# Kernel tuning notes

Measured on AMD Instinct MI355X. Metric: run time of the kernel, lower is better.

The kernel has to match this reference:

```python
import jax, jax.numpy as jnp
import numpy as np

D_MODEL = 1024
D_FF = 4096
NUM_EXPERTS = 8
TOP_K = 2


def setup_inputs() -> dict:
    key = jax.random.key(0)
    ks = jax.random.split(key, 10)
    s = 0.02
    x = jax.random.normal(ks[0], (2, 1024, D_MODEL), dtype=jnp.float32)
    # router gate (nn.Linear(d_model, num_experts))
    Wr = jax.random.normal(ks[1], (D_MODEL, NUM_EXPERTS), dtype=jnp.float32) * s
    br = jnp.zeros((NUM_EXPERTS,), dtype=jnp.float32)
    # stacked expert weights
    Wg = jax.random.normal(ks[2], (NUM_EXPERTS, D_MODEL, D_FF), dtype=jnp.float32) * s
    bg = jnp.zeros((NUM_EXPERTS, D_FF), dtype=jnp.float32)
    Wu = jax.random.normal(ks[3], (NUM_EXPERTS, D_MODEL, D_FF), dtype=jnp.float32) * s
    bu = jnp.zeros((NUM_EXPERTS, D_FF), dtype=jnp.float32)
    Wd = jax.random.normal(ks[4], (NUM_EXPERTS, D_FF, D_MODEL), dtype=jnp.float32) * s
    bd = jnp.zeros((NUM_EXPERTS, D_MODEL), dtype=jnp.float32)
    return {"x": x, "Wr": Wr, "br": br, "Wg": Wg, "bg": bg,
            "Wu": Wu, "bu": bu, "Wd": Wd, "bd": bd}


def reference(x, Wr, br, Wg, bg, Wu, bu, Wd, bd):
    B, S, D = x.shape
    E = Wg.shape[0]
    xt = x.reshape(-1, D)                       # [T, d]
    T = xt.shape[0]
    # router: softmax in float32, top-k, renormalize (Mixtral-style)
    logits = xt @ Wr + br                       # [T, E]
    probs = jax.nn.softmax(logits.astype(jnp.float32), axis=-1)
    rw, sel = jax.lax.top_k(probs, TOP_K)       # [T, K]
    rw = rw / jnp.sum(rw, axis=-1, keepdims=True)
    # per-token per-expert combine weight (0 if expert not selected)
    w_full = jnp.zeros((T, E), dtype=rw.dtype).at[
        jnp.arange(T)[:, None], sel].add(rw)    # [T, E]
    # SwiGLU experts, computed densely over all tokens then masked-combined
    g = jnp.einsum('td,edf->etf', xt, Wg) + bg[:, None, :]   # [E, T, f]
    u = jnp.einsum('td,edf->etf', xt, Wu) + bu[:, None, :]
    h = jax.nn.silu(g) * u
    y = jnp.einsum('etf,efd->etd', h, Wd) + bd[:, None, :]    # [E, T, d]
    out = jnp.einsum('te,etd->td', w_full.astype(x.dtype), y)
    return out.reshape(B, S, D)
```

## Files before the change

kernel.cpp:

```cpp
#include <hip/hip_runtime.h>

typedef float floatx4 __attribute__((ext_vector_type(4)));
typedef __bf16 bf16x2 __attribute__((ext_vector_type(2)));
typedef __bf16 bf16x4 __attribute__((ext_vector_type(4)));
typedef __bf16 bf16x8 __attribute__((ext_vector_type(8)));

#define D_MODEL 1024
#define D_FF 4096
#define NE 8

__device__ __forceinline__ void gload16(const void* g, void* l) {
    __builtin_amdgcn_global_load_lds(
        (const __attribute__((address_space(1))) void*)g,
        (__attribute__((address_space(3))) void*)l, 16, 0, 0);
}

__device__ __forceinline__ int frag_off(int row, int q) {
    return row * 32 + ((q ^ ((row >> 2) & 3)) << 3);
}

__device__ __forceinline__ unsigned int pk(float lo, float hi) {
    union { bf16x2 v; unsigned int u; } c;
    c.v = bf16x2{(__bf16)lo, (__bf16)hi};
    return c.u;
}

__global__ __launch_bounds__(256) void router_kernel(
    const float* __restrict__ x, const float* __restrict__ Wr,
    const float* __restrict__ br, int* __restrict__ cnt,
    int* __restrict__ list, float* __restrict__ w_slot, int T)
{
    int wv = threadIdx.x >> 6;
    int lane = threadIdx.x & 63;
    int t = blockIdx.x * 4 + wv;
    if (t >= T) return;

    const float* xp = x + (size_t)t * D_MODEL;
    float acc[8] = {0.f,0.f,0.f,0.f,0.f,0.f,0.f,0.f};
#pragma unroll
    for (int i = 0; i < 16; ++i) {
        int d = i * 64 + lane;
        float xv = xp[d];
        float4 w0 = *(const float4*)(Wr + d * 8);
        float4 w1 = *(const float4*)(Wr + d * 8 + 4);
        acc[0] += xv * w0.x; acc[1] += xv * w0.y;
        acc[2] += xv * w0.z; acc[3] += xv * w0.w;
        acc[4] += xv * w1.x; acc[5] += xv * w1.y;
        acc[6] += xv * w1.z; acc[7] += xv * w1.w;
    }
#pragma unroll
    for (int off = 32; off >= 1; off >>= 1) {
#pragma unroll
        for (int e = 0; e < 8; ++e)
            acc[e] += __shfl_down(acc[e], off, 64);
    }
    if (lane == 0) {
        float l[8];
#pragma unroll
        for (int e = 0; e < 8; ++e) l[e] = acc[e] + br[e];
        int i0 = 0; float v0 = l[0];
#pragma unroll
        for (int e = 1; e < 8; ++e) if (l[e] > v0) { v0 = l[e]; i0 = e; }
        int i1 = -1; float v1 = -3.4e38f;
#pragma unroll
        for (int e = 0; e < 8; ++e) if (e != i0 && l[e] > v1) { v1 = l[e]; i1 = e; }
        float ex = __expf(v1 - v0);
        float w0 = 1.f / (1.f + ex);
        float w1 = ex / (1.f + ex);
        int p0 = atomicAdd(&cnt[i0], 1);
        list[i0 * T + p0] = 2 * t;
        int p1 = atomicAdd(&cnt[i1], 1);
        list[i1 * T + p1] = 2 * t + 1;
        w_slot[2 * t]     = w0;
        w_slot[2 * t + 1] = w1;
    }
}

__global__ __launch_bounds__(256) void prep_kernel(
    const float* __restrict__ Wg, const float* __restrict__ Wu,
    const float* __restrict__ Wd, const float* __restrict__ x,
    __bf16* __restrict__ Wgt, __bf16* __restrict__ Wut,
    __bf16* __restrict__ Wdt, __bf16* __restrict__ Xb)
{
    const int bid = blockIdx.x;
    const int tid = threadIdx.x;
    if (bid >= 24576) {
        int base = (bid - 24576) * 2048 + tid * 8;
        float4 v0 = *(const float4*)(x + base);
        float4 v1 = *(const float4*)(x + base + 4);
        bf16x8 o = {(__bf16)v0.x, (__bf16)v0.y, (__bf16)v0.z, (__bf16)v0.w,
                    (__bf16)v1.x, (__bf16)v1.y, (__bf16)v1.z, (__bf16)v1.w};
        *(bf16x8*)(Xb + base) = o;
        return;
    }
    const int tensor = bid >> 13;
    const int rem = bid & 8191;
    const int e = rem >> 10;
    const int tile = rem & 1023;
    const float* src; __bf16* dst; int K, N, kb, nb;
    if (tensor == 0)      { src = Wg; dst = Wgt; }
    else if (tensor == 1) { src = Wu; dst = Wut; }
    else                  { src = Wd; dst = Wdt; }
    if (tensor < 2) { K = 1024; N = 4096; kb = (tile & 15) << 6; nb = (tile >> 4) << 6; }
    else            { K = 4096; N = 1024; kb = (tile & 63) << 6; nb = (tile >> 6) << 6; }
    src += (size_t)e * K * N + (size_t)kb * N + nb;
    dst += (size_t)e * K * N + (size_t)nb * K + kb;

    __shared__ unsigned int tp[64 * 33];

    const int p  = tid >> 3;
    const int ci = tid & 7;
    const float* s0 = src + (size_t)(2 * p) * N + 4 * ci;
    float4 r0a = *(const float4*)(s0);
    float4 r0b = *(const float4*)(s0 + 32);
    float4 r1a = *(const float4*)(s0 + N);
    float4 r1b = *(const float4*)(s0 + N + 32);

    unsigned int* w0 = &tp[(4 * ci) * 33 + p];
    w0[0]  = pk(r0a.x, r1a.x);
    w0[33] = pk(r0a.y, r1a.y);
    w0[66] = pk(r0a.z, r1a.z);
    w0[99] = pk(r0a.w, r1a.w);
    unsigned int* w1 = &tp[(4 * ci + 32) * 33 + p];
    w1[0]  = pk(r0b.x, r1b.x);
    w1[33] = pk(r0b.y, r1b.y);
    w1[66] = pk(r0b.z, r1b.z);
    w1[99] = pk(r0b.w, r1b.w);
    __syncthreads();

    const int r = tid >> 2;
    const int q = tid & 3;
    const unsigned int* rp = &tp[r * 33 + q * 8];
    uint4 oa = {rp[0], rp[1], rp[2], rp[3]};
    uint4 ob = {rp[4], rp[5], rp[6], rp[7]};
    __bf16* drow = dst + (size_t)r * K + q * 16;
    *(uint4*)(drow)     = oa;
    *(uint4*)(drow + 8) = ob;
}

__global__ __launch_bounds__(256, 3) void gateup3_kernel(
    const __bf16* __restrict__ Xb, const __bf16* __restrict__ Wgt,
    const __bf16* __restrict__ Wut, const float* __restrict__ bg,
    const float* __restrict__ bu, const int* __restrict__ cnt,
    const int* __restrict__ list, __bf16* __restrict__ H, int T)
{
    const int e  = blockIdx.z;
    const int m0 = blockIdx.y * 128;
    const int n0 = blockIdx.x * 64;
    const int count = cnt[e];
    if (m0 >= count) return;

    __shared__ __bf16 ldsA[8192];
    __shared__ __bf16 ldsBg[4096];
    __shared__ __bf16 ldsBu[4096];
    __shared__ int s_entry[128];

    const int tid = threadIdx.x;
    if (tid < 128) {
        int r = m0 + tid;
        s_entry[tid] = (r < count) ? list[e * T + r] : list[e * T];
    }
    __syncthreads();

    const __bf16* asrc[4]; char* adst[4];
#pragma unroll
    for (int i = 0; i < 4; ++i) {
        int p = i * 256 + tid;
        int s = p >> 9;
        int row = (p & 511) >> 2, j = p & 3;
        int g = j ^ ((row >> 2) & 3);
        asrc[i] = Xb + (size_t)(s_entry[row] >> 1) * D_MODEL + s * 32 + g * 8;
        adst[i] = (char*)ldsA + p * 16;
    }
    const __bf16* gsrc[2]; const __bf16* usrc[2]; char* gdst[2]; char* udst[2];
#pragma unroll
    for (int i = 0; i < 2; ++i) {
        int p = i * 256 + tid;
        int s = p >> 8;
        int row = (p & 255) >> 2, j = p & 3;
        int g = j ^ ((row >> 2) & 3);
        gsrc[i] = Wgt + ((size_t)e * D_FF + n0 + row) * D_MODEL + s * 32 + g * 8;
        usrc[i] = Wut + ((size_t)e * D_FF + n0 + row) * D_MODEL + s * 32 + g * 8;
        gdst[i] = (char*)ldsBg + p * 16;
        udst[i] = (char*)ldsBu + p * 16;
    }

    const int wv = tid >> 6, lane = tid & 63;
    const int wm = wv >> 1, wn = wv & 1;
    const int q = lane >> 4, ln = lane & 15;
    int aoff[4], boff[2];
#pragma unroll
    for (int i = 0; i < 4; ++i) aoff[i] = frag_off(wm * 64 + i * 16 + ln, q);
#pragma unroll
    for (int i = 0; i < 2; ++i) boff[i] = frag_off(wn * 32 + i * 16 + ln, q);

    floatx4 accg[4][2] = {};
    floatx4 accu[4][2] = {};

    for (int k0 = 0; k0 < D_MODEL; k0 += 64) {
#pragma unroll
        for (int i = 0; i < 4; ++i) gload16(asrc[i] + k0, adst[i]);
#pragma unroll
        for (int i = 0; i < 2; ++i) {
            gload16(gsrc[i] + k0, gdst[i]);
            gload16(usrc[i] + k0, udst[i]);
        }
        __syncthreads();

#pragma unroll
        for (int s = 0; s < 2; ++s) {
            bf16x8 af[4], bgf[2], buf[2];
#pragma unroll
            for (int i = 0; i < 4; ++i) af[i]  = *(const bf16x8*)&ldsA[s * 4096 + aoff[i]];
#pragma unroll
            for (int i = 0; i < 2; ++i) bgf[i] = *(const bf16x8*)&ldsBg[s * 2048 + boff[i]];
#pragma unroll
            for (int i = 0; i < 2; ++i) buf[i] = *(const bf16x8*)&ldsBu[s * 2048 + boff[i]];
#pragma unroll
            for (int mi = 0; mi < 4; ++mi)
#pragma unroll
                for (int ni = 0; ni < 2; ++ni) {
                    accg[mi][ni] = __builtin_amdgcn_mfma_f32_16x16x32_bf16(af[mi], bgf[ni], accg[mi][ni], 0, 0, 0);
                    accu[mi][ni] = __builtin_amdgcn_mfma_f32_16x16x32_bf16(af[mi], buf[ni], accu[mi][ni], 0, 0, 0);
                }
        }
        __syncthreads();
    }

#pragma unroll
    for (int ni = 0; ni < 2; ++ni) {
        int col = n0 + wn * 32 + ni * 16 + ln;
        float bgv = bg[e * D_FF + col];
        float buv = bu[e * D_FF + col];
#pragma unroll
        for (int mi = 0; mi < 4; ++mi) {
            int lrow0 = wm * 64 + mi * 16 + q * 4;
#pragma unroll
            for (int r = 0; r < 4; ++r) {
                int lr = lrow0 + r;
                if (m0 + lr < count) {
                    int entry = s_entry[lr];
                    float g = accg[mi][ni][r] + bgv;
                    float u = accu[mi][ni][r] + buv;
                    float h = g / (1.f + __expf(-g)) * u;
                    H[(size_t)entry * D_FF + col] = (__bf16)h;
                }
            }
        }
    }
}

__global__ __launch_bounds__(256, 3) void down3_kernel(
    const __bf16* __restrict__ H, const __bf16* __restrict__ Wdt,
    const float* __restrict__ bd, const int* __restrict__ cnt,
    const int* __restrict__ list, float* __restrict__ Y, int T)
{
    const int e  = blockIdx.z >> 2;
    const int kc = blockIdx.z & 3;
    const int m0 = blockIdx.y * 128;
    const int n0 = blockIdx.x * 128;
    const int count = cnt[e];
    if (m0 >= count) return;

    __shared__ __bf16 ldsA[8192];
    __shared__ __bf16 ldsB[8192];
    __shared__ int s_entry[128];

    const int tid = threadIdx.x;
    if (tid < 128) {
        int r = m0 + tid;
        s_entry[tid] = (r < count) ? list[e * T + r] : list[e * T];
    }
    __syncthreads();

    const int kbase = kc * (D_FF / 4);
    const __bf16* asrc[4]; const __bf16* bsrc[4];
    char* adst[4]; char* bdst[4];
#pragma unroll
    for (int i = 0; i < 4; ++i) {
        int p = i * 256 + tid;
        int s = p >> 9;
        int row = (p & 511) >> 2, j = p & 3;
        int g = j ^ ((row >> 2) & 3);
        asrc[i] = H + (size_t)s_entry[row] * D_FF + kbase + s * 32 + g * 8;
        bsrc[i] = Wdt + ((size_t)e * D_MODEL + n0 + row) * D_FF + kbase + s * 32 + g * 8;
        adst[i] = (char*)ldsA + p * 16;
        bdst[i] = (char*)ldsB + p * 16;
    }

    const int wv = tid >> 6, lane = tid & 63;
    const int wm = wv >> 1, wn = wv & 1;
    const int q = lane >> 4, ln = lane & 15;
    int aoff[4], boff[4];
#pragma unroll
    for (int i = 0; i < 4; ++i) {
        aoff[i] = frag_off(wm * 64 + i * 16 + ln, q);
        boff[i] = frag_off(wn * 64 + i * 16 + ln, q);
    }

    floatx4 acc[4][4] = {};

    for (int k0 = 0; k0 < D_FF / 4; k0 += 64) {
#pragma unroll
        for (int i = 0; i < 4; ++i) {
            gload16(asrc[i] + k0, adst[i]);
            gload16(bsrc[i] + k0, bdst[i]);
        }
        __syncthreads();

#pragma unroll
        for (int s = 0; s < 2; ++s) {
            bf16x8 af[4], bf[4];
#pragma unroll
            for (int i = 0; i < 4; ++i) af[i] = *(const bf16x8*)&ldsA[s * 4096 + aoff[i]];
#pragma unroll
            for (int i = 0; i < 4; ++i) bf[i] = *(const bf16x8*)&ldsB[s * 4096 + boff[i]];
#pragma unroll
            for (int mi = 0; mi < 4; ++mi)
#pragma unroll
                for (int ni = 0; ni < 4; ++ni)
                    acc[mi][ni] = __builtin_amdgcn_mfma_f32_16x16x32_bf16(af[mi], bf[ni], acc[mi][ni], 0, 0, 0);
        }
        __syncthreads();
    }

    const size_t kc_off = (size_t)kc * 2 * T * D_MODEL;
#pragma unroll
    for (int ni = 0; ni < 4; ++ni) {
        int col = n0 + wn * 64 + ni * 16 + ln;
        float bdv = (kc == 0) ? bd[e * D_MODEL + col] : 0.f;
#pragma unroll
        for (int mi = 0; mi < 4; ++mi) {
            int lrow0 = wm * 64 + mi * 16 + q * 4;
#pragma unroll
            for (int r = 0; r < 4; ++r) {
                int lr = lrow0 + r;
                if (m0 + lr < count) {
                    int entry = s_entry[lr];
                    Y[kc_off + (size_t)entry * D_MODEL + col] = acc[mi][ni][r] + bdv;
                }
            }
        }
    }
}

__global__ __launch_bounds__(256) void combine_kernel(
    const float* __restrict__ Y, const float* __restrict__ w_slot,
    float* __restrict__ out, int T)
{
    int idx = blockIdx.x * 256 + threadIdx.x;
    int t = idx >> 8;
    const float4* Y4 = (const float4*)Y;
    size_t r0 = (size_t)(2 * t) * 256 + (idx & 255);
    size_t r1 = r0 + 256;
    size_t ks = (size_t)2 * T * 256;
    float4 a = Y4[r0], b = Y4[r1];
#pragma unroll
    for (int kc = 1; kc < 4; ++kc) {
        float4 va = Y4[r0 + kc * ks], vb = Y4[r1 + kc * ks];
        a.x += va.x; a.y += va.y; a.z += va.z; a.w += va.w;
        b.x += vb.x; b.y += vb.y; b.z += vb.z; b.w += vb.w;
    }
    float w0 = w_slot[2 * t], w1 = w_slot[2 * t + 1];
    float4 o = {w0 * a.x + w1 * b.x, w0 * a.y + w1 * b.y,
                w0 * a.z + w1 * b.z, w0 * a.w + w1 * b.w};
    ((float4*)out)[idx] = o;
}

extern "C" void kernel_launch(void* const* d_in, const int* in_sizes, int n_in,
                              void* d_out, int out_size, void* d_ws, size_t ws_size,
                              hipStream_t stream) {
    const float* x  = (const float*)d_in[0];
    const float* Wr = (const float*)d_in[1];
    const float* br = (const float*)d_in[2];
    const float* Wg = (const float*)d_in[3];
    const float* bg = (const float*)d_in[4];
    const float* Wu = (const float*)d_in[5];
    const float* bu = (const float*)d_in[6];
    const float* Wd = (const float*)d_in[7];
    const float* bd = (const float*)d_in[8];
    float* out = (float*)d_out;
    const int T = in_sizes[0] / D_MODEL;

    char* ws = (char*)d_ws;
    size_t off = 256;
    int*   cnt    = (int*)ws;
    int*   list   = (int*)(ws + off);              off += (size_t)NE * T * 4;
    float* w_slot = (float*)(ws + off);            off += (size_t)2 * T * 4;
    off = (off + 1023) & ~(size_t)1023;
    __bf16* Xb  = (__bf16*)(ws + off);             off += (size_t)T * D_MODEL * 2;
    __bf16* H   = (__bf16*)(ws + off);             off += (size_t)2 * T * D_FF * 2;
    __bf16* Wgt = (__bf16*)(ws + off);
    float*  Y   = (float*)(ws + off);
    off += (size_t)NE * D_MODEL * D_FF * 2;
    __bf16* Wut = (__bf16*)(ws + off);             off += (size_t)NE * D_MODEL * D_FF * 2;
    __bf16* Wdt = (__bf16*)(ws + off);             off += (size_t)NE * D_FF * D_MODEL * 2;

    hipMemsetAsync(cnt, 0, 256, stream);

    router_kernel<<<dim3((T + 3) / 4), dim3(256), 0, stream>>>(x, Wr, br, cnt, list, w_slot, T);

    prep_kernel<<<dim3(25600), dim3(256), 0, stream>>>(Wg, Wu, Wd, x, Wgt, Wut, Wdt, Xb);

    dim3 gb(D_FF / 64, (T + 127) / 128, NE);
    gateup3_kernel<<<gb, dim3(256), 0, stream>>>(Xb, Wgt, Wut, bg, bu, cnt, list, H, T);

    dim3 gc(D_MODEL / 128, (T + 127) / 128, NE * 4);
    down3_kernel<<<gc, dim3(256), 0, stream>>>(H, Wdt, bd, cnt, list, Y, T);

    combine_kernel<<<dim3(T * D_MODEL / 4 / 256), dim3(256), 0, stream>>>(Y, w_slot, out, T);
}
```

Before: 677.2 us.

## Fuse router into prep kernel and overlap Wd transpose with gate/up GEMM

Merges the router kernel into the weight/activation prep kernel so one launch does routing, the Wg/Wu transposes and the x bf16 cast. The Wd transpose moves into extra blocks (z == NE) of the gate/up GEMM grid, each block transposing eight tiles, so this conversion overlaps with the expert GEMM work instead of running before it. This removes a launch and lets memory-bound conversion run alongside compute. The cost is that the extra GEMM blocks compete for CUs and bandwidth, and occupancy is still governed by the GEMM's LDS footprint.

Result: faster. 656.5 us (-3.1%).

```diff
diff --git a/kernel.cpp b/kernel.cpp
--- a/kernel.cpp
+++ b/kernel.cpp
@@ -25,89 +25,10 @@
     return c.u;
 }
 
-__global__ __launch_bounds__(256) void router_kernel(
-    const float* __restrict__ x, const float* __restrict__ Wr,
-    const float* __restrict__ br, int* __restrict__ cnt,
-    int* __restrict__ list, float* __restrict__ w_slot, int T)
+__device__ __forceinline__ void transpose_tile(
+    const float* __restrict__ src, __bf16* __restrict__ dst,
+    int K, int N, unsigned int* tp, int tid)
 {
-    int wv = threadIdx.x >> 6;
-    int lane = threadIdx.x & 63;
-    int t = blockIdx.x * 4 + wv;
-    if (t >= T) return;
-
-    const float* xp = x + (size_t)t * D_MODEL;
-    float acc[8] = {0.f,0.f,0.f,0.f,0.f,0.f,0.f,0.f};
-#pragma unroll
-    for (int i = 0; i < 16; ++i) {
-        int d = i * 64 + lane;
-        float xv = xp[d];
-        float4 w0 = *(const float4*)(Wr + d * 8);
-        float4 w1 = *(const float4*)(Wr + d * 8 + 4);
-        acc[0] += xv * w0.x; acc[1] += xv * w0.y;
-        acc[2] += xv * w0.z; acc[3] += xv * w0.w;
-        acc[4] += xv * w1.x; acc[5] += xv * w1.y;
-        acc[6] += xv * w1.z; acc[7] += xv * w1.w;
-    }
-#pragma unroll
-    for (int off = 32; off >= 1; off >>= 1) {
-#pragma unroll
-        for (int e = 0; e < 8; ++e)
-            acc[e] += __shfl_down(acc[e], off, 64);
-    }
-    if (lane == 0) {
-        float l[8];
-#pragma unroll
-        for (int e = 0; e < 8; ++e) l[e] = acc[e] + br[e];
-        int i0 = 0; float v0 = l[0];
-#pragma unroll
-        for (int e = 1; e < 8; ++e) if (l[e] > v0) { v0 = l[e]; i0 = e; }
-        int i1 = -1; float v1 = -3.4e38f;
-#pragma unroll
-        for (int e = 0; e < 8; ++e) if (e != i0 && l[e] > v1) { v1 = l[e]; i1 = e; }
-        float ex = __expf(v1 - v0);
-        float w0 = 1.f / (1.f + ex);
-        float w1 = ex / (1.f + ex);
-        int p0 = atomicAdd(&cnt[i0], 1);
-        list[i0 * T + p0] = 2 * t;
-        int p1 = atomicAdd(&cnt[i1], 1);
-        list[i1 * T + p1] = 2 * t + 1;
-        w_slot[2 * t]     = w0;
-        w_slot[2 * t + 1] = w1;
-    }
-}
-
-__global__ __launch_bounds__(256) void prep_kernel(
-    const float* __restrict__ Wg, const float* __restrict__ Wu,
-    const float* __restrict__ Wd, const float* __restrict__ x,
-    __bf16* __restrict__ Wgt, __bf16* __restrict__ Wut,
-    __bf16* __restrict__ Wdt, __bf16* __restrict__ Xb)
-{
-    const int bid = blockIdx.x;
-    const int tid = threadIdx.x;
-    if (bid >= 24576) {
-        int base = (bid - 24576) * 2048 + tid * 8;
-        float4 v0 = *(const float4*)(x + base);
-        float4 v1 = *(const float4*)(x + base + 4);
-        bf16x8 o = {(__bf16)v0.x, (__bf16)v0.y, (__bf16)v0.z, (__bf16)v0.w,
-                    (__bf16)v1.x, (__bf16)v1.y, (__bf16)v1.z, (__bf16)v1.w};
-        *(bf16x8*)(Xb + base) = o;
-        return;
-    }
-    const int tensor = bid >> 13;
-    const int rem = bid & 8191;
-    const int e = rem >> 10;
-    const int tile = rem & 1023;
-    const float* src; __bf16* dst; int K, N, kb, nb;
-    if (tensor == 0)      { src = Wg; dst = Wgt; }
-    else if (tensor == 1) { src = Wu; dst = Wut; }
-    else                  { src = Wd; dst = Wdt; }
-    if (tensor < 2) { K = 1024; N = 4096; kb = (tile & 15) << 6; nb = (tile >> 4) << 6; }
-    else            { K = 4096; N = 1024; kb = (tile & 63) << 6; nb = (tile >> 6) << 6; }
-    src += (size_t)e * K * N + (size_t)kb * N + nb;
-    dst += (size_t)e * K * N + (size_t)nb * K + kb;
-
-    __shared__ unsigned int tp[64 * 33];
-
     const int p  = tid >> 3;
     const int ci = tid & 7;
     const float* s0 = src + (size_t)(2 * p) * N + 4 * ci;
@@ -138,24 +59,125 @@
     *(uint4*)(drow + 8) = ob;
 }
 
+__global__ __launch_bounds__(256) void routerprep_kernel(
+    const float* __restrict__ Wg, const float* __restrict__ Wu,
+    const float* __restrict__ x, const float* __restrict__ Wr,
+    const float* __restrict__ br,
+    __bf16* __restrict__ Wgt, __bf16* __restrict__ Wut, __bf16* __restrict__ Xb,
+    int* __restrict__ cnt, int* __restrict__ list, float* __restrict__ w_slot,
+    int T)
+{
+    const int bid = blockIdx.x;
+    const int tid = threadIdx.x;
+
+    if (bid >= 17408) {
+        int wv = tid >> 6;
+        int lane = tid & 63;
+        int t = (bid - 17408) * 4 + wv;
+        if (t >= T) return;
+        const float* xp = x + (size_t)t * D_MODEL;
+        float acc[8] = {0.f,0.f,0.f,0.f,0.f,0.f,0.f,0.f};
+#pragma unroll
+        for (int i = 0; i < 16; ++i) {
+            int d = i * 64 + lane;
+            float xv = xp[d];
+            float4 w0 = *(const float4*)(Wr + d * 8);
+            float4 w1 = *(const float4*)(Wr + d * 8 + 4);
+            acc[0] += xv * w0.x; acc[1] += xv * w0.y;
+            acc[2] += xv * w0.z; acc[3] += xv * w0.w;
+            acc[4] += xv * w1.x; acc[5] += xv * w1.y;
+            acc[6] += xv * w1.z; acc[7] += xv * w1.w;
+        }
+#pragma unroll
+        for (int off = 32; off >= 1; off >>= 1) {
+#pragma unroll
+            for (int e = 0; e < 8; ++e)
+                acc[e] += __shfl_down(acc[e], off, 64);
+        }
+        if (lane == 0) {
+            float l[8];
+#pragma unroll
+            for (int e = 0; e < 8; ++e) l[e] = acc[e] + br[e];
+            int i0 = 0; float v0 = l[0];
+#pragma unroll
+            for (int e = 1; e < 8; ++e) if (l[e] > v0) { v0 = l[e]; i0 = e; }
+            int i1 = -1; float v1 = -3.4e38f;
+#pragma unroll
+            for (int e = 0; e < 8; ++e) if (e != i0 && l[e] > v1) { v1 = l[e]; i1 = e; }
+            float ex = __expf(v1 - v0);
+            float w0 = 1.f / (1.f + ex);
+            float w1 = ex / (1.f + ex);
+            int p0 = atomicAdd(&cnt[i0], 1);
+            list[i0 * T + p0] = 2 * t;
+            int p1 = atomicAdd(&cnt[i1], 1);
+            list[i1 * T + p1] = 2 * t + 1;
+            w_slot[2 * t]     = w0;
+            w_slot[2 * t + 1] = w1;
+        }
+        return;
+    }
+
+    if (bid >= 16384) {
+        int base = (bid - 16384) * 2048 + tid * 8;
+        float4 v0 = *(const float4*)(x + base);
+        float4 v1 = *(const float4*)(x + base + 4);
+        bf16x8 o = {(__bf16)v0.x, (__bf16)v0.y, (__bf16)v0.z, (__bf16)v0.w,
+                    (__bf16)v1.x, (__bf16)v1.y, (__bf16)v1.z, (__bf16)v1.w};
+        *(bf16x8*)(Xb + base) = o;
+        return;
+    }
+
+    __shared__ unsigned int tp[64 * 33];
+    const int tensor = bid >> 13;
+    const int rem = bid & 8191;
+    const int e = rem >> 10;
+    const int tile = rem & 1023;
+    const float* src = (tensor == 0) ? Wg : Wu;
+    __bf16* dst = (tensor == 0) ? Wgt : Wut;
+    const int K = 1024, N = 4096;
+    const int kb = (tile & 15) << 6, nb = (tile >> 4) << 6;
+    src += (size_t)e * K * N + (size_t)kb * N + nb;
+    dst += (size_t)e * K * N + (size_t)nb * K + kb;
+    transpose_tile(src, dst, K, N, tp, tid);
+}
+
 __global__ __launch_bounds__(256, 3) void gateup3_kernel(
     const __bf16* __restrict__ Xb, const __bf16* __restrict__ Wgt,
     const __bf16* __restrict__ Wut, const float* __restrict__ bg,
     const float* __restrict__ bu, const int* __restrict__ cnt,
-    const int* __restrict__ list, __bf16* __restrict__ H, int T)
+    const int* __restrict__ list, __bf16* __restrict__ H,
+    const float* __restrict__ Wd, __bf16* __restrict__ Wdt, int T)
 {
+    __shared__ __bf16 ldsA[8192];
+    __shared__ __bf16 ldsBg[4096];
+    __shared__ __bf16 ldsBu[4096];
+    __shared__ int s_entry[128];
+
+    const int tid = threadIdx.x;
+
+    if (blockIdx.z == NE) {
+        unsigned int* tp = (unsigned int*)ldsA;
+        const int bid2 = blockIdx.y * gridDim.x + blockIdx.x;
+        const int K = 4096, N = 1024;
+#pragma unroll 1
+        for (int i = 0; i < 8; ++i) {
+            if (i) __syncthreads();
+            int tile = bid2 * 8 + i;
+            int e = tile >> 10, tt = tile & 1023;
+            int kb = (tt & 63) << 6, nb = (tt >> 6) << 6;
+            const float* src = Wd + (size_t)e * K * N + (size_t)kb * N + nb;
+            __bf16* dst = Wdt + (size_t)e * K * N + (size_t)nb * K + kb;
+            transpose_tile(src, dst, K, N, tp, tid);
+        }
+        return;
+    }
+
     const int e  = blockIdx.z;
     const int m0 = blockIdx.y * 128;
     const int n0 = blockIdx.x * 64;
     const int count = cnt[e];
     if (m0 >= count) return;
 
-    __shared__ __bf16 ldsA[8192];
-    __shared__ __bf16 ldsBg[4096];
-    __shared__ __bf16 ldsBu[4096];
-    __shared__ int s_entry[128];
-
-    const int tid = threadIdx.x;
     if (tid < 128) {
         int r = m0 + tid;
         s_entry[tid] = (r < count) ? list[e * T + r] : list[e * T];
@@ -398,12 +420,12 @@
 
     hipMemsetAsync(cnt, 0, 256, stream);
 
-    router_kernel<<<dim3((T + 3) / 4), dim3(256), 0, stream>>>(x, Wr, br, cnt, list, w_slot, T);
-
-    prep_kernel<<<dim3(25600), dim3(256), 0, stream>>>(Wg, Wu, Wd, x, Wgt, Wut, Wdt, Xb);
-
-    dim3 gb(D_FF / 64, (T + 127) / 128, NE);
-    gateup3_kernel<<<gb, dim3(256), 0, stream>>>(Xb, Wgt, Wut, bg, bu, cnt, list, H, T);
+    routerprep_kernel<<<dim3(17408 + T / 4), dim3(256), 0, stream>>>(
+        Wg, Wu, x, Wr, br, Wgt, Wut, Xb, cnt, list, w_slot, T);
+
+    dim3 gb(D_FF / 64, (T + 127) / 128, NE + 1);
+    gateup3_kernel<<<gb, dim3(256), 0, stream>>>(
+        Xb, Wgt, Wut, bg, bu, cnt, list, H, Wd, Wdt, T);
 
     dim3 gc(D_MODEL / 128, (T + 127) / 128, NE * 4);
     down3_kernel<<<gc, dim3(256), 0, stream>>>(H, Wdt, bd, cnt, list, Y, T);
```
